# Kernel tuning notes

Measured on AMD Instinct MI355X. Metric: run time of the kernel, lower is better.

The kernel has to match this reference:

```python
import jax, jax.numpy as jnp
import numpy as np

D_MODEL = 1024
N_HEADS = 16
DK = D_MODEL // N_HEADS


def setup_inputs() -> dict:
    key = jax.random.key(0)
    k1, k2, k3, k4 = jax.random.split(key, 4)
    x = jax.random.normal(k1, (2, 2048, D_MODEL), dtype=jnp.float32)
    # torch nn.Linear stores weight as [out_features, in_features]
    W_qkv = jax.random.normal(k2, (3 * D_MODEL, D_MODEL), dtype=jnp.float32) * (1.0 / np.sqrt(D_MODEL))
    W_proj = jax.random.normal(k3, (D_MODEL, D_MODEL), dtype=jnp.float32) * (1.0 / np.sqrt(D_MODEL))
    b_proj = jax.random.normal(k4, (D_MODEL,), dtype=jnp.float32) * 0.01
    return {"x": x, "W_qkv": W_qkv, "W_proj": W_proj, "b_proj": b_proj}


def reference(x, W_qkv, W_proj, b_proj):
    B, L, D = x.shape
    qkv = x @ W_qkv.T                      # [B, L, 3D]
    q, k, v = jnp.split(qkv, 3, axis=-1)   # each [B, L, D]

    def split_heads(t):
        return t.reshape(B, L, N_HEADS, DK).transpose(0, 2, 1, 3)  # [B, H, L, dk]

    q, k, v = map(split_heads, (q, k, v))
    scale = jnp.float32(1.0 / np.sqrt(DK))
    scores = jnp.einsum('bhid,bhjd->bhij', q, k) * scale  # [B, H, L, L]
    attn = jax.nn.softmax(scores, axis=-1)
    out = jnp.einsum('bhij,bhjd->bhid', attn, v)           # [B, H, L, dk]
    out = out.transpose(0, 2, 1, 3).reshape(B, L, D)
    return out @ W_proj.T + b_proj
```

## Files before the change

### kernel.cpp

```cpp
#include <hip/hip_runtime.h>
#include <stdint.h>

typedef unsigned short ushort_t;
typedef __bf16 bf16x4 __attribute__((ext_vector_type(4)));
typedef __bf16 bf16x8 __attribute__((ext_vector_type(8)));
typedef float f32x4 __attribute__((ext_vector_type(4)));
typedef float f32x16 __attribute__((ext_vector_type(16)));
typedef unsigned short us8 __attribute__((ext_vector_type(8)));
typedef unsigned short us4v __attribute__((ext_vector_type(4)));

__device__ __forceinline__ float bf2f(ushort_t u) {
  union { uint32_t u; float f; } v; v.u = ((uint32_t)u) << 16; return v.f;
}
__device__ __forceinline__ ushort_t f2bf(float f) {
  union { float f; uint32_t u; } v; v.f = f;
  uint32_t u = v.u;
  uint32_t r = (u + 0x7FFFu + ((u >> 16) & 1u)) >> 16;
  return (ushort_t)r;
}
__device__ __forceinline__ uint32_t cvtpk(float a, float b) {
  uint32_t r;
  asm("v_cvt_pk_bf16_f32 %0, %1, %2" : "=v"(r) : "v"(a), "v"(b));
  return r;
}
__device__ __forceinline__ void gload_lds16(const void* g, void* l) {
  __builtin_amdgcn_global_load_lds(
      (const __attribute__((address_space(1))) void*)g,
      (__attribute__((address_space(3))) void*)l, 16, 0, 0);
}
__device__ __forceinline__ void tr2(const ushort_t* p, bf16x4& lo, bf16x4& hi) {
  asm volatile("ds_read_b64_tr_b16 %0, %2\n\t"
               "ds_read_b64_tr_b16 %1, %2 offset:128"
               : "=&v"(lo), "=&v"(hi)
               : "v"((const __attribute__((address_space(3))) ushort_t*)p));
}

template <typename T> __device__ __forceinline__ T to_out(float f);
template <> __device__ __forceinline__ ushort_t to_out<ushort_t>(float f) { return f2bf(f); }
template <> __device__ __forceinline__ float to_out<float>(float f) { return f; }

#define SCQ 0.1803368801111204f

__global__ void f2b3_kernel(const float* __restrict__ a, ushort_t* __restrict__ ao,
                            const float* __restrict__ b, ushort_t* __restrict__ bo,
                            const float* __restrict__ c, ushort_t* __restrict__ co) {
  int blk = blockIdx.x;
  const float* src; ushort_t* dst; int n4, b0, nb;
  if (blk < 1024)      { src = a; dst = ao; n4 = 1048576; b0 = blk;        nb = 1024; }
  else if (blk < 1792) { src = b; dst = bo; n4 = 786432;  b0 = blk - 1024; nb = 768; }
  else                 { src = c; dst = co; n4 = 262144;  b0 = blk - 1792; nb = 256; }
  for (int i = b0 * 256 + threadIdx.x; i < n4; i += nb * 256) {
    float4 v = ((const float4*)src)[i];
    us4v o;
    o[0] = f2bf(v.x); o[1] = f2bf(v.y); o[2] = f2bf(v.z); o[3] = f2bf(v.w);
    ((us4v*)dst)[i] = o;
  }
}

template<bool BIAS, typename OT, bool SCALEQ>
__global__ __launch_bounds__(256, 2) void gemm_bt(
    const ushort_t* __restrict__ A, const ushort_t* __restrict__ W,
    const float* __restrict__ bias, OT* __restrict__ C,
    int M, int N, int K)
{
  __shared__ ushort_t As[128 * 64];
  __shared__ ushort_t Bs[128 * 64];
  const int t = threadIdx.x;
  const int w = t >> 6, lane = t & 63;
  const int lg = lane >> 4, lc = lane & 15;

  const int NX = N >> 7;
  const int nwg = gridDim.x;
  const int o = blockIdx.x;
  const int id = (o & 7) * (nwg >> 3) + (o >> 3);
  const int rowbase = (id / NX) * 128;
  const int colbase = (id % NX) * 128;
  const int wr = (w >> 1) * 64, wc = (w & 1) * 64;

  f32x4 acc[4][4] = {};
  const int nkt = K >> 6;

  for (int kt = 0; kt < nkt; ++kt) {
#pragma unroll
    for (int i = 0; i < 4; ++i) {
      int off = (i * 256 + t) * 16;
      int row = off >> 7;
      int cb  = off & 127;
      int ec  = cb ^ ((row & 7) << 4);
      gload_lds16(A + (size_t)(rowbase + row) * K + kt * 64 + (ec >> 1),
                  (char*)As + off);
      gload_lds16(W + (size_t)(colbase + row) * K + kt * 64 + (ec >> 1),
                  (char*)Bs + off);
    }
    __syncthreads();
#pragma unroll
    for (int kk = 0; kk < 2; ++kk) {
      bf16x8 af[4], bf[4];
#pragma unroll
      for (int m = 0; m < 4; ++m) {
        int row = wr + m * 16 + lc;
        int kb  = (lg * 16 + kk * 64) ^ ((row & 7) << 4);
        af[m] = *(const bf16x8*)((const char*)As + row * 128 + kb);
        int col = wc + m * 16 + lc;
        int kb2 = (lg * 16 + kk * 64) ^ ((col & 7) << 4);
        bf[m] = *(const bf16x8*)((const char*)Bs + col * 128 + kb2);
      }
#pragma unroll
      for (int m = 0; m < 4; ++m)
#pragma unroll
        for (int n = 0; n < 4; ++n)
          acc[m][n] = __builtin_amdgcn_mfma_f32_16x16x32_bf16(af[m], bf[n],
                                                              acc[m][n], 0, 0, 0);
    }
    __syncthreads();
  }

#pragma unroll
  for (int m = 0; m < 4; ++m) {
    int r0 = rowbase + wr + m * 16 + lg * 4;
#pragma unroll
    for (int n = 0; n < 4; ++n) {
      int c0 = colbase + wc + n * 16 + lc;
      float bv = 0.f;
      if (BIAS) bv = bias[c0];
      float qs = 1.f;
      if (SCALEQ) qs = (c0 < 1024) ? SCQ : 1.f;
#pragma unroll
      for (int j = 0; j < 4; ++j)
        C[(size_t)(r0 + j) * N + c0] = to_out<OT>(acc[m][n][j] * qs + bv);
    }
  }
}

__global__ __launch_bounds__(512, 4) void attn_fwd(
    const ushort_t* __restrict__ qkv, ushort_t* __restrict__ o1,
    ushort_t* __restrict__ o2, float* __restrict__ lbuf)
{
  __shared__ ushort_t Ks[2][64 * 64];
  __shared__ ushort_t Vs[2][64 * 64];

  const int t = threadIdx.x, w = t >> 6, lane = t & 63;
  const int l31 = lane & 31, hi = lane >> 5;
  const int lc = lane & 15;

  const int d = blockIdx.x;
  const int qt = (d >> 3) & 7;
  const int bhs = (d & 7) * 8 + (d >> 6);
  const int bh = bhs >> 1, split = bhs & 1;
  const int b = bh >> 4, h = bh & 15;

  const ushort_t* Qg = qkv + (size_t)(b * 2048) * 3072 + h * 64;
  const ushort_t* Kg = Qg + 1024 + (size_t)split * 1024 * 3072;
  const ushort_t* Vg = Qg + 2048 + (size_t)split * 1024 * 3072;

  auto stage_k = [&](ushort_t* Kd, int kt) {
    int off = t * 16;
    int row = off >> 7;
    int cb  = off & 127;
    int ec  = cb ^ ((row & 7) << 4);
    gload_lds16(Kg + (size_t)(kt * 64 + row) * 3072 + (ec >> 1),
                (char*)Kd + off);
  };
  const int vr  = t >> 3;
  const int vc0 = (t & 7) * 8;
  const int vdst = (vc0 >> 4) * 2048 + (vr >> 2) * 128 + (vr & 3) * 32 +
                   (vc0 & 8) * 2;

  const ushort_t* qrow_p = Qg + (size_t)(qt * 256 + w * 32 + l31) * 3072;
  bf16x8 qf[4];
#pragma unroll
  for (int kk = 0; kk < 4; ++kk)
    qf[kk] = *(const bf16x8*)(qrow_p + kk * 16 + hi * 8);

  bf16x8 ones;
#pragma unroll
  for (int i = 0; i < 8; ++i) ones[i] = (__bf16)1.0f;

  stage_k(Ks[0], 0);
  {
    us8 v = *(const us8*)(Vg + (size_t)vr * 3072 + vc0);
    *(us8*)((char*)Vs[0] + vdst) = v;
  }
  __syncthreads();

  f32x16 oacc0 = {}, oacc1 = {}, lacc = {};
  const int m16 = (lane >> 4) & 1;

  int cur = 0;
  for (int kt = 0; kt < 16; ++kt) {
    us8 vnext;
    if (kt < 15) {
      stage_k(Ks[cur ^ 1], kt + 1);
      vnext = *(const us8*)(Vg + (size_t)((kt + 1) * 64 + vr) * 3072 + vc0);
    }

    const ushort_t* Kc = Ks[cur];
    f32x16 s0 = {}, s1 = {};
    __builtin_amdgcn_s_setprio(1);
#pragma unroll
    for (int kk = 0; kk < 4; ++kk) {
      int cbyte = (kk * 32 + hi * 16);
      int r0 = l31, r1 = 32 + l31;
      bf16x8 kf0 = *(const bf16x8*)((const char*)Kc + r0 * 128 +
                                    (cbyte ^ ((r0 & 7) << 4)));
      bf16x8 kf1 = *(const bf16x8*)((const char*)Kc + r1 * 128 +
                                    (cbyte ^ ((r1 & 7) << 4)));
      s0 = __builtin_amdgcn_mfma_f32_32x32x16_bf16(kf0, qf[kk], s0, 0, 0, 0);
      s1 = __builtin_amdgcn_mfma_f32_32x32x16_bf16(kf1, qf[kk], s1, 0, 0, 0);
    }
    __builtin_amdgcn_s_setprio(0);

#pragma unroll
    for (int i = 0; i < 16; ++i) {
      s0[i] = __builtin_amdgcn_exp2f(s0[i]);
      s1[i] = __builtin_amdgcn_exp2f(s1[i]);
    }

    uint32_t pk0[8], pk1[8];
#pragma unroll
    for (int j = 0; j < 8; ++j) {
      pk0[j] = cvtpk(s0[2 * j], s0[2 * j + 1]);
      pk1[j] = cvtpk(s1[2 * j], s1[2 * j + 1]);
    }

    if (kt < 15)
      *(us8*)((char*)Vs[cur ^ 1] + vdst) = vnext;

    const ushort_t* Vc = Vs[cur];
    bf16x8 pa[4], vf[4][2];
#pragma unroll
    for (int ks = 0; ks < 4; ++ks) {
      int j0 = 4 * (ks & 1);
      uint32_t x0 = (ks < 2) ? pk0[j0]     : pk1[j0];
      uint32_t x1 = (ks < 2) ? pk0[j0 + 1] : pk1[j0 + 1];
      uint32_t y0 = (ks < 2) ? pk0[j0 + 2] : pk1[j0 + 2];
      uint32_t y1 = (ks < 2) ? pk0[j0 + 3] : pk1[j0 + 3];
      asm volatile("v_permlane32_swap_b32 %0, %1" : "+v"(x0), "+v"(y0));
      asm volatile("v_permlane32_swap_b32 %0, %1" : "+v"(x1), "+v"(y1));
      union { uint32_t du[4]; bf16x8 v; } U;
      U.du[0] = x0; U.du[1] = x1; U.du[2] = y0; U.du[3] = y1;
      pa[ks] = U.v;
#pragma unroll
      for (int nd = 0; nd < 2; ++nd) {
        bf16x4 lo, hh;
        tr2(Vc + (nd * 2 + m16) * 1024 + (4 * ks + 2 * hi) * 64 + lc * 4, lo, hh);
        vf[ks][nd] = __builtin_shufflevector(lo, hh, 0, 1, 2, 3, 4, 5, 6, 7);
      }
    }
    asm volatile("s_waitcnt lgkmcnt(0)" ::: "memory");
    __builtin_amdgcn_sched_barrier(0);
    __builtin_amdgcn_s_setprio(1);
#pragma unroll
    for (int ks = 0; ks < 4; ++ks) {
      oacc0 = __builtin_amdgcn_mfma_f32_32x32x16_bf16(pa[ks], vf[ks][0], oacc0, 0, 0, 0);
      oacc1 = __builtin_amdgcn_mfma_f32_32x32x16_bf16(pa[ks], vf[ks][1], oacc1, 0, 0, 0);
      lacc  = __builtin_amdgcn_mfma_f32_32x32x16_bf16(pa[ks], ones, lacc, 0, 0, 0);
    }
    __builtin_amdgcn_s_setprio(0);

    __syncthreads();
    cur ^= 1;
  }

  ushort_t* op = split ? o2 : o1;
  const int qrow0 = qt * 256 + w * 32;
#pragma unroll
  for (int r = 0; r < 16; ++r) {
    int crow = (r & 3) + 8 * (r >> 2) + 4 * hi;
    size_t base = ((size_t)(b * 2048 + qrow0 + crow)) * 1024 + h * 64 + l31;
    op[base]      = f2bf(oacc0[r]);
    op[base + 32] = f2bf(oacc1[r]);
  }
  if (l31 == 0) {
#pragma unroll
    for (int r = 0; r < 16; ++r) {
      int crow = (r & 3) + 8 * (r >> 2) + 4 * hi;
      lbuf[(size_t)split * 65536 +
           (size_t)(b * 2048 + qrow0 + crow) * 16 + h] = lacc[r];
    }
  }
}

__global__ void merge_kernel(ushort_t* __restrict__ o1,
                             const ushort_t* __restrict__ o2,
                             const float* __restrict__ lbuf) {
  int i = blockIdx.x * blockDim.x + threadIdx.x;
  int row = i >> 7;
  int col = (i & 127) * 8;
  int h = col >> 6;
  float l1 = lbuf[(size_t)row * 16 + h];
  float l2 = lbuf[65536 + (size_t)row * 16 + h];
  float inv = 1.f / (l1 + l2);
  us8 v1 = ((const us8*)o1)[i];
  us8 v2 = ((const us8*)o2)[i];
  us8 o;
#pragma unroll
  for (int j = 0; j < 8; ++j)
    o[j] = f2bf((bf2f(v1[j]) + bf2f(v2[j])) * inv);
  ((us8*)o1)[i] = o;
}

extern "C" void kernel_launch(void* const* d_in, const int* in_sizes, int n_in,
                              void* d_out, int out_size, void* d_ws, size_t ws_size,
                              hipStream_t stream) {
  const float* x     = (const float*)d_in[0];
  const float* Wqkv  = (const float*)d_in[1];
  const float* Wproj = (const float*)d_in[2];
  const float* bproj = (const float*)d_in[3];
  float* out = (float*)d_out;

  ushort_t* qkv   = (ushort_t*)d_ws;
  ushort_t* o1    = qkv   + (size_t)4096 * 3072;
  ushort_t* xb    = o1    + (size_t)4096 * 1024;
  ushort_t* wqb   = xb    + (size_t)4096 * 1024;
  ushort_t* wpb   = wqb   + (size_t)3072 * 1024;
  float*    lbuf  = (float*)(wpb + (size_t)1024 * 1024);

  dim3 blk(256);
  f2b3_kernel<<<2048, blk, 0, stream>>>(x, xb, Wqkv, wqb, Wproj, wpb);

  gemm_bt<false, ushort_t, true><<<768, blk, 0, stream>>>(
      xb, wqb, nullptr, qkv, 4096, 3072, 1024);
  attn_fwd<<<dim3(512), dim3(512), 0, stream>>>(qkv, o1, xb, lbuf);
  merge_kernel<<<2048, blk, 0, stream>>>(o1, xb, lbuf);
  gemm_bt<true, float, false><<<256, blk, 0, stream>>>(
      o1, wpb, bproj, out, 4096, 1024, 1024);
}
```

Before: 109.2 us.

## Process two query tiles per wave and compute row sums with VALU adds

The attention kernel now uses 256-thread blocks in which each wave handles 64 query rows (two 32-row tiles) instead of 32. Each K and V fragment read from LDS is therefore reused across twice as many MFMAs, and each thread stages twice as many K/V elements. The softmax denominator is now built from VALU adds of the exponentials plus a cross-half shuffle, replacing the extra MFMA against a ones vector. The costs are more registers per wave, fewer waves to hide latency, and different launch bounds.

```diff
diff --git a/kernel.cpp b/kernel.cpp
--- a/kernel.cpp
+++ b/kernel.cpp
@@ -132,7 +132,7 @@
   }
 }
 
-__global__ __launch_bounds__(512, 4) void attn_fwd(
+__global__ __launch_bounds__(256, 2) void attn_fwd(
     const ushort_t* __restrict__ qkv, ushort_t* __restrict__ o1,
     ushort_t* __restrict__ o2, float* __restrict__ lbuf)
 {
@@ -142,6 +142,7 @@
   const int t = threadIdx.x, w = t >> 6, lane = t & 63;
   const int l31 = lane & 31, hi = lane >> 5;
   const int lc = lane & 15;
+  const int m16 = (lane >> 4) & 1;
 
   const int d = blockIdx.x;
   const int qt = (d >> 3) & 7;
@@ -154,48 +155,58 @@
   const ushort_t* Vg = Qg + 2048 + (size_t)split * 1024 * 3072;
 
   auto stage_k = [&](ushort_t* Kd, int kt) {
-    int off = t * 16;
-    int row = off >> 7;
-    int cb  = off & 127;
-    int ec  = cb ^ ((row & 7) << 4);
-    gload_lds16(Kg + (size_t)(kt * 64 + row) * 3072 + (ec >> 1),
-                (char*)Kd + off);
+#pragma unroll
+    for (int i = 0; i < 2; ++i) {
+      int off = (i * 256 + t) * 16;
+      int row = off >> 7;
+      int cb  = off & 127;
+      int ec  = cb ^ ((row & 7) << 4);
+      gload_lds16(Kg + (size_t)(kt * 64 + row) * 3072 + (ec >> 1),
+                  (char*)Kd + off);
+    }
   };
-  const int vr  = t >> 3;
-  const int vc0 = (t & 7) * 8;
-  const int vdst = (vc0 >> 4) * 2048 + (vr >> 2) * 128 + (vr & 3) * 32 +
-                   (vc0 & 8) * 2;
-
-  const ushort_t* qrow_p = Qg + (size_t)(qt * 256 + w * 32 + l31) * 3072;
-  bf16x8 qf[4];
-#pragma unroll
-  for (int kk = 0; kk < 4; ++kk)
-    qf[kk] = *(const bf16x8*)(qrow_p + kk * 16 + hi * 8);
-
-  bf16x8 ones;
-#pragma unroll
-  for (int i = 0; i < 8; ++i) ones[i] = (__bf16)1.0f;
+  int vr[2], vc0[2], vdst[2];
+#pragma unroll
+  for (int i = 0; i < 2; ++i) {
+    int u = i * 256 + t;
+    vr[i]  = u >> 3;
+    vc0[i] = (u & 7) * 8;
+    vdst[i] = (vc0[i] >> 4) * 2048 + (vr[i] >> 2) * 128 + (vr[i] & 3) * 32 +
+              (vc0[i] & 8) * 2;
+  }
+
+  const ushort_t* qpA = Qg + (size_t)(qt * 256 + w * 64 + l31) * 3072;
+  const ushort_t* qpB = qpA + (size_t)32 * 3072;
+  bf16x8 qfA[4], qfB[4];
+#pragma unroll
+  for (int kk = 0; kk < 4; ++kk) {
+    qfA[kk] = *(const bf16x8*)(qpA + kk * 16 + hi * 8);
+    qfB[kk] = *(const bf16x8*)(qpB + kk * 16 + hi * 8);
+  }
 
   stage_k(Ks[0], 0);
-  {
-    us8 v = *(const us8*)(Vg + (size_t)vr * 3072 + vc0);
-    *(us8*)((char*)Vs[0] + vdst) = v;
+#pragma unroll
+  for (int i = 0; i < 2; ++i) {
+    us8 v = *(const us8*)(Vg + (size_t)vr[i] * 3072 + vc0[i]);
+    *(us8*)((char*)Vs[0] + vdst[i]) = v;
   }
   __syncthreads();
 
-  f32x16 oacc0 = {}, oacc1 = {}, lacc = {};
-  const int m16 = (lane >> 4) & 1;
+  f32x16 oA0 = {}, oA1 = {}, oB0 = {}, oB1 = {};
+  float lA = 0.f, lB = 0.f;
 
   int cur = 0;
   for (int kt = 0; kt < 16; ++kt) {
-    us8 vnext;
+    us8 vnext[2];
     if (kt < 15) {
       stage_k(Ks[cur ^ 1], kt + 1);
-      vnext = *(const us8*)(Vg + (size_t)((kt + 1) * 64 + vr) * 3072 + vc0);
+#pragma unroll
+      for (int i = 0; i < 2; ++i)
+        vnext[i] = *(const us8*)(Vg + (size_t)((kt + 1) * 64 + vr[i]) * 3072 + vc0[i]);
     }
 
     const ushort_t* Kc = Ks[cur];
-    f32x16 s0 = {}, s1 = {};
+    f32x16 sA0 = {}, sA1 = {}, sB0 = {}, sB1 = {};
     __builtin_amdgcn_s_setprio(1);
 #pragma unroll
     for (int kk = 0; kk < 4; ++kk) {
@@ -205,56 +216,109 @@
                                     (cbyte ^ ((r0 & 7) << 4)));
       bf16x8 kf1 = *(const bf16x8*)((const char*)Kc + r1 * 128 +
                                     (cbyte ^ ((r1 & 7) << 4)));
-      s0 = __builtin_amdgcn_mfma_f32_32x32x16_bf16(kf0, qf[kk], s0, 0, 0, 0);
-      s1 = __builtin_amdgcn_mfma_f32_32x32x16_bf16(kf1, qf[kk], s1, 0, 0, 0);
+      sA0 = __builtin_amdgcn_mfma_f32_32x32x16_bf16(kf0, qfA[kk], sA0, 0, 0, 0);
+      sA1 = __builtin_amdgcn_mfma_f32_32x32x16_bf16(kf1, qfA[kk], sA1, 0, 0, 0);
+      sB0 = __builtin_amdgcn_mfma_f32_32x32x16_bf16(kf0, qfB[kk], sB0, 0, 0, 0);
+      sB1 = __builtin_amdgcn_mfma_f32_32x32x16_bf16(kf1, qfB[kk], sB1, 0, 0, 0);
     }
     __builtin_amdgcn_s_setprio(0);
 
-#pragma unroll
-    for (int i = 0; i < 16; ++i) {
-      s0[i] = __builtin_amdgcn_exp2f(s0[i]);
-      s1[i] = __builtin_amdgcn_exp2f(s1[i]);
-    }
-
-    uint32_t pk0[8], pk1[8];
-#pragma unroll
-    for (int j = 0; j < 8; ++j) {
-      pk0[j] = cvtpk(s0[2 * j], s0[2 * j + 1]);
-      pk1[j] = cvtpk(s1[2 * j], s1[2 * j + 1]);
-    }
-
-    if (kt < 15)
-      *(us8*)((char*)Vs[cur ^ 1] + vdst) = vnext;
-
     const ushort_t* Vc = Vs[cur];
-    bf16x8 pa[4], vf[4][2];
-#pragma unroll
-    for (int ks = 0; ks < 4; ++ks) {
-      int j0 = 4 * (ks & 1);
-      uint32_t x0 = (ks < 2) ? pk0[j0]     : pk1[j0];
-      uint32_t x1 = (ks < 2) ? pk0[j0 + 1] : pk1[j0 + 1];
-      uint32_t y0 = (ks < 2) ? pk0[j0 + 2] : pk1[j0 + 2];
-      uint32_t y1 = (ks < 2) ? pk0[j0 + 3] : pk1[j0 + 3];
-      asm volatile("v_permlane32_swap_b32 %0, %1" : "+v"(x0), "+v"(y0));
-      asm volatile("v_permlane32_swap_b32 %0, %1" : "+v"(x1), "+v"(y1));
-      union { uint32_t du[4]; bf16x8 v; } U;
-      U.du[0] = x0; U.du[1] = x1; U.du[2] = y0; U.du[3] = y1;
-      pa[ks] = U.v;
+    bf16x8 vf[4][2];
+#pragma unroll
+    for (int ks = 0; ks < 4; ++ks)
 #pragma unroll
       for (int nd = 0; nd < 2; ++nd) {
         bf16x4 lo, hh;
         tr2(Vc + (nd * 2 + m16) * 1024 + (4 * ks + 2 * hi) * 64 + lc * 4, lo, hh);
         vf[ks][nd] = __builtin_shufflevector(lo, hh, 0, 1, 2, 3, 4, 5, 6, 7);
       }
-    }
+
+    bf16x8 paA[4], paB[4];
+    {
+#pragma unroll
+      for (int i = 0; i < 16; ++i) {
+        sA0[i] = __builtin_amdgcn_exp2f(sA0[i]);
+        sA1[i] = __builtin_amdgcn_exp2f(sA1[i]);
+      }
+      lA += ((((sA0[0] + sA0[1]) + (sA0[2] + sA0[3])) +
+              ((sA0[4] + sA0[5]) + (sA0[6] + sA0[7]))) +
+             (((sA0[8] + sA0[9]) + (sA0[10] + sA0[11])) +
+              ((sA0[12] + sA0[13]) + (sA0[14] + sA0[15])))) +
+            ((((sA1[0] + sA1[1]) + (sA1[2] + sA1[3])) +
+              ((sA1[4] + sA1[5]) + (sA1[6] + sA1[7]))) +
+             (((sA1[8] + sA1[9]) + (sA1[10] + sA1[11])) +
+              ((sA1[12] + sA1[13]) + (sA1[14] + sA1[15]))));
+      uint32_t pk0[8], pk1[8];
+#pragma unroll
+      for (int j = 0; j < 8; ++j) {
+        pk0[j] = cvtpk(sA0[2 * j], sA0[2 * j + 1]);
+        pk1[j] = cvtpk(sA1[2 * j], sA1[2 * j + 1]);
+      }
+#pragma unroll
+      for (int ks = 0; ks < 4; ++ks) {
+        int j0 = 4 * (ks & 1);
+        uint32_t x0 = (ks < 2) ? pk0[j0]     : pk1[j0];
+        uint32_t x1 = (ks < 2) ? pk0[j0 + 1] : pk1[j0 + 1];
+        uint32_t y0 = (ks < 2) ? pk0[j0 + 2] : pk1[j0 + 2];
+        uint32_t y1 = (ks < 2) ? pk0[j0 + 3] : pk1[j0 + 3];
+        asm volatile("v_permlane32_swap_b32 %0, %1" : "+v"(x0), "+v"(y0));
+        asm volatile("v_permlane32_swap_b32 %0, %1" : "+v"(x1), "+v"(y1));
+        union { uint32_t du[4]; bf16x8 v; } U;
+        U.du[0] = x0; U.du[1] = x1; U.du[2] = y0; U.du[3] = y1;
+        paA[ks] = U.v;
+      }
+    }
+    {
+#pragma unroll
+      for (int i = 0; i < 16; ++i) {
+        sB0[i] = __builtin_amdgcn_exp2f(sB0[i]);
+        sB1[i] = __builtin_amdgcn_exp2f(sB1[i]);
+      }
+      lB += ((((sB0[0] + sB0[1]) + (sB0[2] + sB0[3])) +
+              ((sB0[4] + sB0[5]) + (sB0[6] + sB0[7]))) +
+             (((sB0[8] + sB0[9]) + (sB0[10] + sB0[11])) +
+              ((sB0[12] + sB0[13]) + (sB0[14] + sB0[15])))) +
+            ((((sB1[0] + sB1[1]) + (sB1[2] + sB1[3])) +
+              ((sB1[4] + sB1[5]) + (sB1[6] + sB1[7]))) +
+             (((sB1[8] + sB1[9]) + (sB1[10] + sB1[11])) +
+              ((sB1[12] + sB1[13]) + (sB1[14] + sB1[15]))));
+      uint32_t pk0[8], pk1[8];
+#pragma unroll
+      for (int j = 0; j < 8; ++j) {
+        pk0[j] = cvtpk(sB0[2 * j], sB0[2 * j + 1]);
+        pk1[j] = cvtpk(sB1[2 * j], sB1[2 * j + 1]);
+      }
+#pragma unroll
+      for (int ks = 0; ks < 4; ++ks) {
+        int j0 = 4 * (ks & 1);
+        uint32_t x0 = (ks < 2) ? pk0[j0]     : pk1[j0];
+        uint32_t x1 = (ks < 2) ? pk0[j0 + 1] : pk1[j0 + 1];
+        uint32_t y0 = (ks < 2) ? pk0[j0 + 2] : pk1[j0 + 2];
+        uint32_t y1 = (ks < 2) ? pk0[j0 + 3] : pk1[j0 + 3];
+        asm volatile("v_permlane32_swap_b32 %0, %1" : "+v"(x0), "+v"(y0));
+        asm volatile("v_permlane32_swap_b32 %0, %1" : "+v"(x1), "+v"(y1));
+        union { uint32_t du[4]; bf16x8 v; } U;
+        U.du[0] = x0; U.du[1] = x1; U.du[2] = y0; U.du[3] = y1;
+        paB[ks] = U.v;
+      }
+    }
+
+    if (kt < 15) {
+#pragma unroll
+      for (int i = 0; i < 2; ++i)
+        *(us8*)((char*)Vs[cur ^ 1] + vdst[i]) = vnext[i];
+    }
+
     asm volatile("s_waitcnt lgkmcnt(0)" ::: "memory");
     __builtin_amdgcn_sched_barrier(0);
     __builtin_amdgcn_s_setprio(1);
 #pragma unroll
     for (int ks = 0; ks < 4; ++ks) {
-      oacc0 = __builtin_amdgcn_mfma_f32_32x32x16_bf16(pa[ks], vf[ks][0], oacc0, 0, 0, 0);
-      oacc1 = __builtin_amdgcn_mfma_f32_32x32x16_bf16(pa[ks], vf[ks][1], oacc1, 0, 0, 0);
-      lacc  = __builtin_amdgcn_mfma_f32_32x32x16_bf16(pa[ks], ones, lacc, 0, 0, 0);
+      oA0 = __builtin_amdgcn_mfma_f32_32x32x16_bf16(paA[ks], vf[ks][0], oA0, 0, 0, 0);
+      oA1 = __builtin_amdgcn_mfma_f32_32x32x16_bf16(paA[ks], vf[ks][1], oA1, 0, 0, 0);
+      oB0 = __builtin_amdgcn_mfma_f32_32x32x16_bf16(paB[ks], vf[ks][0], oB0, 0, 0, 0);
+      oB1 = __builtin_amdgcn_mfma_f32_32x32x16_bf16(paB[ks], vf[ks][1], oB1, 0, 0, 0);
     }
     __builtin_amdgcn_s_setprio(0);
 
@@ -262,22 +326,24 @@
     cur ^= 1;
   }
 
+  lA += __shfl_xor(lA, 32);
+  lB += __shfl_xor(lB, 32);
+
   ushort_t* op = split ? o2 : o1;
-  const int qrow0 = qt * 256 + w * 32;
+  const int q0 = qt * 256 + w * 64;
 #pragma unroll
   for (int r = 0; r < 16; ++r) {
     int crow = (r & 3) + 8 * (r >> 2) + 4 * hi;
-    size_t base = ((size_t)(b * 2048 + qrow0 + crow)) * 1024 + h * 64 + l31;
-    op[base]      = f2bf(oacc0[r]);
-    op[base + 32] = f2bf(oacc1[r]);
-  }
-  if (l31 == 0) {
-#pragma unroll
-    for (int r = 0; r < 16; ++r) {
-      int crow = (r & 3) + 8 * (r >> 2) + 4 * hi;
-      lbuf[(size_t)split * 65536 +
-           (size_t)(b * 2048 + qrow0 + crow) * 16 + h] = lacc[r];
-    }
+    size_t baseA = ((size_t)(b * 2048 + q0 + crow)) * 1024 + h * 64 + l31;
+    size_t baseB = baseA + (size_t)32 * 1024;
+    op[baseA]      = f2bf(oA0[r]);
+    op[baseA + 32] = f2bf(oA1[r]);
+    op[baseB]      = f2bf(oB0[r]);
+    op[baseB + 32] = f2bf(oB1[r]);
+  }
+  if (hi == 0) {
+    lbuf[(size_t)split * 65536 + (size_t)(b * 2048 + q0 + l31) * 16 + h] = lA;
+    lbuf[(size_t)split * 65536 + (size_t)(b * 2048 + q0 + 32 + l31) * 16 + h] = lB;
   }
 }
 
@@ -321,7 +387,7 @@
 
   gemm_bt<false, ushort_t, true><<<768, blk, 0, stream>>>(
       xb, wqb, nullptr, qkv, 4096, 3072, 1024);
-  attn_fwd<<<dim3(512), dim3(512), 0, stream>>>(qkv, o1, xb, lbuf);
+  attn_fwd<<<dim3(512), dim3(256), 0, stream>>>(qkv, o1, xb, lbuf);
   merge_kernel<<<2048, blk, 0, stream>>>(o1, xb, lbuf);
   gemm_bt<true, float, false><<<256, blk, 0, stream>>>(
       o1, wpb, bproj, out, 4096, 1024, 1024);
```

New measurement: 109.5 us. No clear change (+0.3%).

## Replace QKV GEMM with 256x256-tile 8-wave kernel using 4-stage LDS pipeline

Applied to the files above, without the earlier changes.

Adds a dedicated QKV projection GEMM that gives each 512-thread block a 256x256 output tile. It stages half-K slices through a 4-deep swizzled LDS ring using direct global-to-LDS loads, interleaved with MFMA phases, barriers and priority hints. The larger tile improves operand reuse and cuts global traffic per FLOP. The cost is that only 192 blocks launch, fewer than the CU count on MI355X, which leaves some CUs idle, and the output is still written with scalar bf16 stores.

```diff
diff --git a/kernel.cpp b/kernel.cpp
--- a/kernel.cpp
+++ b/kernel.cpp
@@ -40,6 +40,7 @@
 template <> __device__ __forceinline__ float to_out<float>(float f) { return f; }
 
 #define SCQ 0.1803368801111204f
+#define VMCNT(n) asm volatile("s_waitcnt vmcnt(" #n ")" ::: "memory")
 
 __global__ void f2b3_kernel(const float* __restrict__ a, ushort_t* __restrict__ ao,
                             const float* __restrict__ b, ushort_t* __restrict__ bo,
@@ -57,6 +58,163 @@
   }
 }
 
+__global__ __launch_bounds__(512, 1) void gemm256_qkv(
+    const ushort_t* __restrict__ A, const ushort_t* __restrict__ W,
+    ushort_t* __restrict__ C)
+{
+  __shared__ ushort_t Lds[4 * 16384];
+
+  const int t = threadIdx.x;
+  const int w = t >> 6, lane = t & 63;
+  const int lg = lane >> 4, lc = lane & 15;
+  const int wr = w >> 2, wc = w & 3;
+
+  const int o = blockIdx.x;
+  const int id = (o & 7) * 24 + (o >> 3);
+  const int rowbase = (id / 12) * 256;
+  const int colbase = (id % 12) * 256;
+
+  auto stageA = [&](int h) {
+    int kt2 = h >> 1, kh = h & 1;
+    char* db = (char*)Lds + (h & 3) * 32768;
+#pragma unroll
+    for (int g = 0; g < 2; ++g) {
+      int r = (t >> 2) + g * 128;
+      int cs = (t & 3) ^ (r & 3);
+      gload_lds16(A + (size_t)(rowbase + r) * 1024 + kt2 * 64 + kh * 32 + cs * 8,
+                  db + g * 8192 + t * 16);
+    }
+  };
+  auto stageB = [&](int h) {
+    int kt2 = h >> 1, kh = h & 1;
+    char* db = (char*)Lds + (h & 3) * 32768 + 16384;
+#pragma unroll
+    for (int g = 0; g < 2; ++g) {
+      int r = (t >> 2) + g * 128;
+      int cs = (t & 3) ^ (r & 3);
+      gload_lds16(W + (size_t)(colbase + r) * 1024 + kt2 * 64 + kh * 32 + cs * 8,
+                  db + g * 8192 + t * 16);
+    }
+  };
+
+  f32x4 acc[8][4] = {};
+
+  stageA(0); stageB(0);
+  stageA(1); stageB(1);
+  stageA(2); stageB(2);
+  VMCNT(8);
+  __builtin_amdgcn_s_barrier();
+
+  for (int kt = 0; kt < 16; ++kt) {
+    const int s0 = (2 * kt) & 3;
+    const ushort_t* A0p = Lds + s0 * 16384;
+    const ushort_t* B0p = A0p + 8192;
+    const ushort_t* A1p = Lds + (s0 + 1) * 16384;
+    const ushort_t* B1p = A1p + 8192;
+
+    bf16x8 bf[4], af[4];
+
+#pragma unroll
+    for (int n = 0; n < 4; ++n) {
+      int row = wc * 64 + n * 16 + lc;
+      bf[n] = *(const bf16x8*)((const char*)B0p + row * 64 +
+                               ((lg ^ (row & 3)) << 4));
+    }
+#pragma unroll
+    for (int m = 0; m < 4; ++m) {
+      int row = wr * 128 + m * 16 + lc;
+      af[m] = *(const bf16x8*)((const char*)A0p + row * 64 +
+                               ((lg ^ (row & 3)) << 4));
+    }
+    if (kt < 15) stageA(2 * kt + 3);
+    __builtin_amdgcn_s_barrier();
+    __builtin_amdgcn_s_setprio(1);
+#pragma unroll
+    for (int m = 0; m < 4; ++m)
+#pragma unroll
+      for (int n = 0; n < 4; ++n)
+        acc[m][n] = __builtin_amdgcn_mfma_f32_16x16x32_bf16(af[m], bf[n],
+                                                            acc[m][n], 0, 0, 0);
+    __builtin_amdgcn_s_setprio(0);
+    __builtin_amdgcn_s_barrier();
+
+#pragma unroll
+    for (int m = 0; m < 4; ++m) {
+      int row = wr * 128 + (m + 4) * 16 + lc;
+      af[m] = *(const bf16x8*)((const char*)A0p + row * 64 +
+                               ((lg ^ (row & 3)) << 4));
+    }
+    if (kt < 15) stageB(2 * kt + 3);
+    __builtin_amdgcn_s_barrier();
+    __builtin_amdgcn_s_setprio(1);
+#pragma unroll
+    for (int m = 0; m < 4; ++m)
+#pragma unroll
+      for (int n = 0; n < 4; ++n)
+        acc[m + 4][n] = __builtin_amdgcn_mfma_f32_16x16x32_bf16(af[m], bf[n],
+                                                                acc[m + 4][n], 0, 0, 0);
+    __builtin_amdgcn_s_setprio(0);
+    if (kt < 15) { VMCNT(8); } else { VMCNT(0); }
+    __builtin_amdgcn_s_barrier();
+
+#pragma unroll
+    for (int n = 0; n < 4; ++n) {
+      int row = wc * 64 + n * 16 + lc;
+      bf[n] = *(const bf16x8*)((const char*)B1p + row * 64 +
+                               ((lg ^ (row & 3)) << 4));
+    }
+#pragma unroll
+    for (int m = 0; m < 4; ++m) {
+      int row = wr * 128 + m * 16 + lc;
+      af[m] = *(const bf16x8*)((const char*)A1p + row * 64 +
+                               ((lg ^ (row & 3)) << 4));
+    }
+    if (kt < 14) stageA(2 * kt + 4);
+    __builtin_amdgcn_s_barrier();
+    __builtin_amdgcn_s_setprio(1);
+#pragma unroll
+    for (int m = 0; m < 4; ++m)
+#pragma unroll
+      for (int n = 0; n < 4; ++n)
+        acc[m][n] = __builtin_amdgcn_mfma_f32_16x16x32_bf16(af[m], bf[n],
+                                                            acc[m][n], 0, 0, 0);
+    __builtin_amdgcn_s_setprio(0);
+    __builtin_amdgcn_s_barrier();
+
+#pragma unroll
+    for (int m = 0; m < 4; ++m) {
+      int row = wr * 128 + (m + 4) * 16 + lc;
+      af[m] = *(const bf16x8*)((const char*)A1p + row * 64 +
+                               ((lg ^ (row & 3)) << 4));
+    }
+    if (kt < 14) stageB(2 * kt + 4);
+    __builtin_amdgcn_s_barrier();
+    __builtin_amdgcn_s_setprio(1);
+#pragma unroll
+    for (int m = 0; m < 4; ++m)
+#pragma unroll
+      for (int n = 0; n < 4; ++n)
+        acc[m + 4][n] = __builtin_amdgcn_mfma_f32_16x16x32_bf16(af[m], bf[n],
+                                                                acc[m + 4][n], 0, 0, 0);
+    __builtin_amdgcn_s_setprio(0);
+    if (kt < 14)      { VMCNT(8); __builtin_amdgcn_s_barrier(); }
+    else if (kt == 14){ VMCNT(4); __builtin_amdgcn_s_barrier(); }
+  }
+
+#pragma unroll
+  for (int m = 0; m < 8; ++m) {
+    int r0 = rowbase + wr * 128 + m * 16 + lg * 4;
+#pragma unroll
+    for (int n = 0; n < 4; ++n) {
+      int c0 = colbase + wc * 64 + n * 16 + lc;
+      float qs = (c0 < 1024) ? SCQ : 1.f;
+#pragma unroll
+      for (int j = 0; j < 4; ++j)
+        C[(size_t)(r0 + j) * 3072 + c0] = f2bf(acc[m][n][j] * qs);
+    }
+  }
+}
+
 template<bool BIAS, typename OT, bool SCALEQ>
 __global__ __launch_bounds__(256, 2) void gemm_bt(
     const ushort_t* __restrict__ A, const ushort_t* __restrict__ W,
@@ -319,8 +477,7 @@
   dim3 blk(256);
   f2b3_kernel<<<2048, blk, 0, stream>>>(x, xb, Wqkv, wqb, Wproj, wpb);
 
-  gemm_bt<false, ushort_t, true><<<768, blk, 0, stream>>>(
-      xb, wqb, nullptr, qkv, 4096, 3072, 1024);
+  gemm256_qkv<<<192, dim3(512), 0, stream>>>(xb, wqb, qkv);
   attn_fwd<<<dim3(512), dim3(512), 0, stream>>>(qkv, o1, xb, lbuf);
   merge_kernel<<<2048, blk, 0, stream>>>(o1, xb, lbuf);
   gemm_bt<true, float, false><<<256, blk, 0, stream>>>(
```

After: 115.7 us. 1.06x slower.
